# Kernel optimization log

Hardware: AMD Instinct MI355X
Metric: run time of the kernel (lower is better)

## Reference

```python
import jax, jax.numpy as jnp
import numpy as np

N = 50000
IN_DIM = 128
HID = 16
HEADS = 8
NUM_CLASSES = 16
NEG_SLOPE = 0.2


def _glorot(key, shape):
    fan_in, fan_out = shape[0], shape[-1]
    lim = float(np.sqrt(6.0 / (fan_in + fan_out)))
    return jax.random.uniform(key, shape, jnp.float32, -lim, lim)


def setup_inputs() -> dict:
    key = jax.random.key(0)
    ks = jax.random.split(key, 12)
    x = jax.random.normal(ks[0], (N, IN_DIM), jnp.float32)
    edge_index = jax.random.randint(ks[1], (2, 1600000), 0, N, jnp.int64)
    # conv1: in=IN_DIM, out per head=HID, heads=HEADS
    Wl1 = _glorot(ks[2], (IN_DIM, HEADS * HID))
    Wr1 = _glorot(ks[3], (IN_DIM, HEADS * HID))
    att1 = _glorot(ks[4], (HEADS, HID))
    b1 = jnp.zeros((HEADS * HID,), jnp.float32)
    # conv2: in=HID*HEADS, out per head=NUM_CLASSES
    Wl2 = _glorot(ks[5], (HEADS * HID, HEADS * NUM_CLASSES))
    Wr2 = _glorot(ks[6], (HEADS * HID, HEADS * NUM_CLASSES))
    att2 = _glorot(ks[7], (HEADS, NUM_CLASSES))
    b2 = jnp.zeros((HEADS * NUM_CLASSES,), jnp.float32)
    # final linear: NUM_CLASSES*HEADS -> NUM_CLASSES
    Wlin = _glorot(ks[8], (HEADS * NUM_CLASSES, NUM_CLASSES))
    blin = jnp.zeros((NUM_CLASSES,), jnp.float32)
    return dict(x=x, edge_index=edge_index, Wl1=Wl1, Wr1=Wr1, att1=att1, b1=b1,
                Wl2=Wl2, Wr2=Wr2, att2=att2, b2=b2, Wlin=Wlin, blin=blin)


def _gatv2_conv(x, src, dst, Wl, Wr, att, bias, heads, out_ch):
    n = x.shape[0]
    xl = (x @ Wl).reshape(n, heads, out_ch)  # source transform
    xr = (x @ Wr).reshape(n, heads, out_ch)  # target transform
    # additive attention logits per edge (GATv2)
    e = jax.nn.leaky_relu(xl[src] + xr[dst], NEG_SLOPE)          # [E,H,C]
    logits = jnp.einsum('ehc,hc->eh', e, att)                     # [E,H]
    # per-destination segment softmax
    m = jax.ops.segment_max(logits, dst, num_segments=n)          # [N,H]
    a = jnp.exp(logits - m[dst])                                  # [E,H]
    s = jax.ops.segment_sum(a, dst, num_segments=n)               # [N,H]
    alpha = a / (s[dst] + 1e-16)
    out = jax.ops.segment_sum(alpha[:, :, None] * xl[src], dst, num_segments=n)
    return out.reshape(n, heads * out_ch) + bias


def reference(x, edge_index, Wl1, Wr1, att1, b1, Wl2, Wr2, att2, b2, Wlin, blin):
    n = x.shape[0]
    # add self-loops (PyG GATv2Conv default add_self_loops=True)
    loop = jnp.arange(n, dtype=edge_index.dtype)
    src = jnp.concatenate([edge_index[0], loop])
    dst = jnp.concatenate([edge_index[1], loop])
    h = _gatv2_conv(x, src, dst, Wl1, Wr1, att1, b1, HEADS, HID)
    h = jax.nn.relu(h)  # dropout identity in eval mode
    h = _gatv2_conv(h, src, dst, Wl2, Wr2, att2, b2, HEADS, NUM_CLASSES)
    h = jax.nn.relu(h)
    logits = h @ Wlin + blin
    return jax.nn.log_softmax(logits, axis=1)
```

## Files before the change

### kernel.cpp

```cpp
#include <hip/hip_runtime.h>

#define HEADS 8
#define FDIM 128
#define NCLS 16
#define NEG_SLOPE 0.2f
#define LOG2E 1.4426950408889634f

typedef __attribute__((ext_vector_type(8))) short bf16x8;
typedef __attribute__((ext_vector_type(4))) float f32x4;

__device__ __forceinline__ unsigned short f2bf(float f) {
    unsigned u = __float_as_uint(f);
    unsigned r = u + 0x7FFFu + ((u >> 16) & 1u);
    return (unsigned short)(r >> 16);
}

__global__ __launch_bounds__(256) void gemm_csr(const float* __restrict__ X,
                                                const float* __restrict__ W0,
                                                const float* __restrict__ W1,
                                                unsigned short* __restrict__ Y0,
                                                unsigned short* __restrict__ Y1,
                                                int n,
                                                const int* __restrict__ srcs,
                                                const int* __restrict__ dsts,
                                                int* __restrict__ cnt,
                                                int* __restrict__ adj,
                                                int E0, int pad, int S) {
    __shared__ __align__(16) unsigned short xs[4 * 4 * 64 * 8];
    __shared__ __align__(16) unsigned short ws[8 * 4 * 64 * 8];
    const int t = threadIdx.x;
    const int x = blockIdx.x;
    int gIdx;
    if (S > 0) {
        if ((x % 3) == 2) {
            int i = (x / 3) * 256 + t;
            const int stride = S * 256;
            for (; i < E0; i += stride) {
                const int d = dsts[i];
                const int rk = atomicAdd(&cnt[d], 1);
                if (rk < pad) adj[(size_t)d * pad + rk] = srcs[i];
            }
            return;
        }
        gIdx = (x / 3) * 2 + (x % 3);
    } else {
        gIdx = x;
    }
    const int Gh = (n + 63) >> 6;
    if (gIdx >= 2 * Gh) return;
    const float* W = (gIdx < Gh) ? W0 : W1;
    unsigned short* Y = (gIdx < Gh) ? Y0 : Y1;
    const int nb = (gIdx < Gh ? gIdx : gIdx - Gh) * 64;

#pragma unroll
    for (int i = 0; i < 8; i++) {
        const int f = t + i * 256;
        const int node = f >> 5, k4 = f & 31;
        float4 v = make_float4(0.f, 0.f, 0.f, 0.f);
        if (nb + node < n) v = ((const float4*)(X + (size_t)(nb + node) * 128))[k4];
        const int kc = k4 >> 3;
        const int q = (k4 & 7) >> 1;
        const int half = k4 & 1;
        const int lane = q * 16 + (node & 15);
        const int w_ = node >> 4;
        union { unsigned short us[4]; uint2 u2; } pk;
        pk.us[0] = f2bf(v.x); pk.us[1] = f2bf(v.y);
        pk.us[2] = f2bf(v.z); pk.us[3] = f2bf(v.w);
        *(uint2*)&xs[(((w_ * 4 + kc) * 64 + lane) << 3) + half * 4] = pk.u2;
    }
#pragma unroll
    for (int i = 0; i < 16; i++) {
        const int f = t + i * 256;
        const int k = f >> 5, n4 = f & 31;
        const float4 v = *(const float4*)(W + k * 128 + n4 * 4);
        const int kc = k >> 5, q = (k >> 3) & 3, j = k & 7;
        const float vv[4] = {v.x, v.y, v.z, v.w};
#pragma unroll
        for (int e = 0; e < 4; e++) {
            const int nn = n4 * 4 + e;
            const int ct = nn >> 4;
            const int lane = q * 16 + (nn & 15);
            ws[(((ct * 4 + kc) * 64 + lane) << 3) + j] = f2bf(vv[e]);
        }
    }
    __syncthreads();

    const int w = t >> 6, lane = t & 63;
    f32x4 acc[8];
#pragma unroll
    for (int i = 0; i < 8; i++) acc[i] = (f32x4){0.f, 0.f, 0.f, 0.f};
    const bf16x8* xa = (const bf16x8*)xs;
    const bf16x8* wb = (const bf16x8*)ws;
#pragma unroll
    for (int kc = 0; kc < 4; kc++) {
        const bf16x8 a = xa[(w * 4 + kc) * 64 + lane];
#pragma unroll
        for (int ct = 0; ct < 8; ct++) {
            const bf16x8 b = wb[(ct * 4 + kc) * 64 + lane];
            acc[ct] = __builtin_amdgcn_mfma_f32_16x16x32_bf16(a, b, acc[ct], 0, 0, 0);
        }
    }
    const int q = lane >> 4, nn = lane & 15;
#pragma unroll
    for (int ct = 0; ct < 8; ct++) {
#pragma unroll
        for (int r = 0; r < 4; r++) {
            const int row = nb + w * 16 + q * 4 + r;
            if (row < n) Y[(size_t)row * 128 + ct * 16 + nn] = f2bf(acc[ct][r]);
        }
    }
}

__global__ __launch_bounds__(256) void node_gather(const unsigned short* __restrict__ xl,
                                                   const unsigned short* __restrict__ xr,
                                                   const float* __restrict__ att,
                                                   const int* __restrict__ adj,
                                                   const int* __restrict__ cnt,
                                                   const float* __restrict__ bias,
                                                   float* __restrict__ outC,
                                                   const float* __restrict__ headW,
                                                   const float* __restrict__ headB,
                                                   float* __restrict__ outH,
                                                   int n, int pad) {
    __shared__ float WsL[FDIM * NCLS];
    __shared__ __align__(16) float stage[4][FDIM];
    const int t = threadIdx.x;
    if (headW) {
        for (int i = t; i < FDIM * NCLS; i += 256) WsL[i] = headW[i];
        __syncthreads();
    }
    const int lane = t & 63;
    const int w = t >> 6;
    const int node = blockIdx.x * 4 + w;
    if (node >= n) return;
    const int half = lane >> 5;
    const int sub = lane & 31;
    const int col = sub * 4;
    const float4 av = *(const float4*)(att + col);
    const float a0 = av.x * LOG2E, a1 = av.y * LOG2E;
    const float a2 = av.z * LOG2E, a3 = av.w * LOG2E;

    float r0, r1, r2, r3, sl0, sl1, sl2, sl3;
    {
        const uint2 rv = *(const uint2*)(xr + (size_t)node * FDIM + col);
        r0 = __uint_as_float(rv.x << 16); r1 = __uint_as_float(rv.x & 0xFFFF0000u);
        r2 = __uint_as_float(rv.y << 16); r3 = __uint_as_float(rv.y & 0xFFFF0000u);
        const uint2 lv = *(const uint2*)(xl + (size_t)node * FDIM + col);
        sl0 = __uint_as_float(lv.x << 16); sl1 = __uint_as_float(lv.x & 0xFFFF0000u);
        sl2 = __uint_as_float(lv.y << 16); sl3 = __uint_as_float(lv.y & 0xFFFF0000u);
    }
    float mx;
    {
        float z0 = sl0 + r0; z0 = fmaxf(z0, NEG_SLOPE * z0);
        float z1 = sl1 + r1; z1 = fmaxf(z1, NEG_SLOPE * z1);
        float z2 = sl2 + r2; z2 = fmaxf(z2, NEG_SLOPE * z2);
        float z3 = sl3 + r3; z3 = fmaxf(z3, NEG_SLOPE * z3);
        float p = z0 * a0 + z1 * a1 + z2 * a2 + z3 * a3;
        p += __shfl_xor(p, 1, 64);
        p += __shfl_xor(p, 2, 64);
        mx = p;
    }
    float s, acc0, acc1, acc2, acc3;
    if (half == 0) { s = 1.f; acc0 = sl0; acc1 = sl1; acc2 = sl2; acc3 = sl3; }
    else           { s = 0.f; acc0 = acc1 = acc2 = acc3 = 0.f; }

    const int* ap = adj + (size_t)node * pad;
    const int deg = min(cnt[node], pad);
    int j = 0;
    for (; j + 8 <= deg; j += 8) {
        const int4 sa = *(const int4*)(ap + j);
        const int4 sb = *(const int4*)(ap + j + 4);
#pragma unroll
        for (int k = 0; k < 4; k++) {
            int pA, pB;
            if (k == 0) { pA = sa.x; pB = sa.y; }
            else if (k == 1) { pA = sa.z; pB = sa.w; }
            else if (k == 2) { pA = sb.x; pB = sb.y; }
            else { pA = sb.z; pB = sb.w; }
            const int src = half ? pB : pA;
            const uint2 lv = *(const uint2*)(xl + (size_t)src * FDIM + col);
            const float l0 = __uint_as_float(lv.x << 16);
            const float l1 = __uint_as_float(lv.x & 0xFFFF0000u);
            const float l2 = __uint_as_float(lv.y << 16);
            const float l3 = __uint_as_float(lv.y & 0xFFFF0000u);
            float z0 = l0 + r0; z0 = fmaxf(z0, NEG_SLOPE * z0);
            float z1 = l1 + r1; z1 = fmaxf(z1, NEG_SLOPE * z1);
            float z2 = l2 + r2; z2 = fmaxf(z2, NEG_SLOPE * z2);
            float z3 = l3 + r3; z3 = fmaxf(z3, NEG_SLOPE * z3);
            float p = z0 * a0 + z1 * a1 + z2 * a2 + z3 * a3;
            p += __shfl_xor(p, 1, 64);
            p += __shfl_xor(p, 2, 64);
            const float e = exp2f(p - mx);
            s += e;
            acc0 += e * l0; acc1 += e * l1; acc2 += e * l2; acc3 += e * l3;
        }
    }
    for (; j < deg; j += 2) {
        const int pA = ap[j];
        const int pB = (j + 1 < deg) ? ap[j + 1] : pA;
        const float gate = (half == 0 || j + 1 < deg) ? 1.f : 0.f;
        const int src = half ? pB : pA;
        const uint2 lv = *(const uint2*)(xl + (size_t)src * FDIM + col);
        const float l0 = __uint_as_float(lv.x << 16);
        const float l1 = __uint_as_float(lv.x & 0xFFFF0000u);
        const float l2 = __uint_as_float(lv.y << 16);
        const float l3 = __uint_as_float(lv.y & 0xFFFF0000u);
        float z0 = l0 + r0; z0 = fmaxf(z0, NEG_SLOPE * z0);
        float z1 = l1 + r1; z1 = fmaxf(z1, NEG_SLOPE * z1);
        float z2 = l2 + r2; z2 = fmaxf(z2, NEG_SLOPE * z2);
        float z3 = l3 + r3; z3 = fmaxf(z3, NEG_SLOPE * z3);
        float p = z0 * a0 + z1 * a1 + z2 * a2 + z3 * a3;
        p += __shfl_xor(p, 1, 64);
        p += __shfl_xor(p, 2, 64);
        const float e = exp2f(p - mx) * gate;
        s += e;
        acc0 += e * l0; acc1 += e * l1; acc2 += e * l2; acc3 += e * l3;
    }
    s    += __shfl_xor(s, 32, 64);
    acc0 += __shfl_xor(acc0, 32, 64);
    acc1 += __shfl_xor(acc1, 32, 64);
    acc2 += __shfl_xor(acc2, 32, 64);
    acc3 += __shfl_xor(acc3, 32, 64);

    const float inv = 1.f / (s + 1e-16f);
    const float4 bv = *(const float4*)(bias + col);
    float o0 = fmaxf(acc0 * inv + bv.x, 0.f);
    float o1 = fmaxf(acc1 * inv + bv.y, 0.f);
    float o2 = fmaxf(acc2 * inv + bv.z, 0.f);
    float o3 = fmaxf(acc3 * inv + bv.w, 0.f);

    if (!headW) {
        if (half == 0)
            *(float4*)(outC + (size_t)node * FDIM + col) = make_float4(o0, o1, o2, o3);
        return;
    }
    if (half == 0)
        *(float4*)&stage[w][col] = make_float4(o0, o1, o2, o3);
    const int cls = lane & 15;
    const int q = lane >> 4;
    float acc = 0.f;
#pragma unroll
    for (int k = 0; k < 32; k++)
        acc += stage[w][q * 32 + k] * WsL[(q * 32 + k) * NCLS + cls];
    acc += __shfl_xor(acc, 16, 64);
    acc += __shfl_xor(acc, 32, 64);
    acc += headB[cls];
    float m2 = acc;
    m2 = fmaxf(m2, __shfl_xor(m2, 8, 64));
    m2 = fmaxf(m2, __shfl_xor(m2, 4, 64));
    m2 = fmaxf(m2, __shfl_xor(m2, 2, 64));
    m2 = fmaxf(m2, __shfl_xor(m2, 1, 64));
    float sm = __expf(acc - m2);
    sm += __shfl_xor(sm, 8, 64);
    sm += __shfl_xor(sm, 4, 64);
    sm += __shfl_xor(sm, 2, 64);
    sm += __shfl_xor(sm, 1, 64);
    if (lane < 16)
        outH[(size_t)node * NCLS + cls] = acc - m2 - __logf(sm);
}

extern "C" void kernel_launch(void* const* d_in, const int* in_sizes, int n_in,
                              void* d_out, int out_size, void* d_ws, size_t ws_size,
                              hipStream_t stream) {
    const float* x    = (const float*)d_in[0];
    const int*   edge = (const int*)d_in[1];
    const float* Wl1  = (const float*)d_in[2];
    const float* Wr1  = (const float*)d_in[3];
    const float* att1 = (const float*)d_in[4];
    const float* b1   = (const float*)d_in[5];
    const float* Wl2  = (const float*)d_in[6];
    const float* Wr2  = (const float*)d_in[7];
    const float* att2 = (const float*)d_in[8];
    const float* b2   = (const float*)d_in[9];
    const float* Wlin = (const float*)d_in[10];
    const float* blin = (const float*)d_in[11];

    const int N = in_sizes[0] / FDIM;
    const int E0 = in_sizes[1] / 2;
    const int* srcs = edge;
    const int* dsts = edge + E0;

    int PAD = 96;
    {
        size_t need = (size_t)N * FDIM * 2 * 2 + (size_t)N * FDIM * 4
                    + (size_t)N * 4 + (size_t)N * PAD * 4;
        if (need > ws_size) PAD = 72;
    }

    unsigned short* A = (unsigned short*)d_ws;
    unsigned short* B = A + (size_t)N * FDIM;
    float* C   = (float*)(B + (size_t)N * FDIM);
    int* cnt   = (int*)(C + (size_t)N * FDIM);
    int* adj   = cnt + N;

    const int Gh = (N + 63) / 64;
    const int G = 2 * Gh;
    const int node_blocks = (N + 3) / 4;

    hipMemsetAsync(cnt, 0, (size_t)N * sizeof(int), stream);

    gemm_csr<<<3 * Gh, 256, 0, stream>>>(
        x, Wl1, Wr1, A, B, N, srcs, dsts, cnt, adj, E0, PAD, Gh);
    node_gather<<<node_blocks, 256, 0, stream>>>(A, B, att1, adj, cnt, b1, C,
                                                 nullptr, nullptr, nullptr, N, PAD);

    gemm_csr<<<G, 256, 0, stream>>>(
        C, Wl2, Wr2, A, B, N, nullptr, nullptr, nullptr, nullptr, 0, PAD, 0);
    node_gather<<<node_blocks, 256, 0, stream>>>(A, B, att2, adj, cnt, b2,
                                                 nullptr, Wlin, blin,
                                                 (float*)d_out, N, PAD);
}
```

Measured before the change: 396.5 us.

## Persistent GEMM blocks, direct A-fragment loads, bf16 hidden layer, dual accumulators

The GEMM kernel becomes persistent: a fixed grid of blocks loads and converts W into shared memory once, then loops over node tiles, loading A fragments straight from global memory into registers instead of staging them in shared memory. The CSR build uses its own fixed set of blocks. The layer-1 output is stored as bf16, which halves its write and read traffic, and the layer-2 GEMM reads that bf16 directly. The gather loop splits into two independent accumulator sets to add ILP. The cost is more rounding from the bf16 intermediate and less parallelism per tile in the GEMM.

New measurement: 394.8 us. Within noise of the previous version (-0.4%).

```diff
diff --git a/kernel.cpp b/kernel.cpp
--- a/kernel.cpp
+++ b/kernel.cpp
@@ -15,7 +15,8 @@
     return (unsigned short)(r >> 16);
 }
 
-__global__ __launch_bounds__(256) void gemm_csr(const float* __restrict__ X,
+__global__ __launch_bounds__(256) void gemm_csr(const float* __restrict__ Xf,
+                                                const unsigned short* __restrict__ Xb,
                                                 const float* __restrict__ W0,
                                                 const float* __restrict__ W1,
                                                 unsigned short* __restrict__ Y0,
@@ -25,49 +26,24 @@
                                                 const int* __restrict__ dsts,
                                                 int* __restrict__ cnt,
                                                 int* __restrict__ adj,
-                                                int E0, int pad, int S) {
-    __shared__ __align__(16) unsigned short xs[4 * 4 * 64 * 8];
+                                                int E0, int pad, int GB, int SB) {
     __shared__ __align__(16) unsigned short ws[8 * 4 * 64 * 8];
     const int t = threadIdx.x;
     const int x = blockIdx.x;
-    int gIdx;
-    if (S > 0) {
-        if ((x % 3) == 2) {
-            int i = (x / 3) * 256 + t;
-            const int stride = S * 256;
-            for (; i < E0; i += stride) {
-                const int d = dsts[i];
-                const int rk = atomicAdd(&cnt[d], 1);
-                if (rk < pad) adj[(size_t)d * pad + rk] = srcs[i];
-            }
-            return;
-        }
-        gIdx = (x / 3) * 2 + (x % 3);
-    } else {
-        gIdx = x;
-    }
-    const int Gh = (n + 63) >> 6;
-    if (gIdx >= 2 * Gh) return;
-    const float* W = (gIdx < Gh) ? W0 : W1;
-    unsigned short* Y = (gIdx < Gh) ? Y0 : Y1;
-    const int nb = (gIdx < Gh ? gIdx : gIdx - Gh) * 64;
-
-#pragma unroll
-    for (int i = 0; i < 8; i++) {
-        const int f = t + i * 256;
-        const int node = f >> 5, k4 = f & 31;
-        float4 v = make_float4(0.f, 0.f, 0.f, 0.f);
-        if (nb + node < n) v = ((const float4*)(X + (size_t)(nb + node) * 128))[k4];
-        const int kc = k4 >> 3;
-        const int q = (k4 & 7) >> 1;
-        const int half = k4 & 1;
-        const int lane = q * 16 + (node & 15);
-        const int w_ = node >> 4;
-        union { unsigned short us[4]; uint2 u2; } pk;
-        pk.us[0] = f2bf(v.x); pk.us[1] = f2bf(v.y);
-        pk.us[2] = f2bf(v.z); pk.us[3] = f2bf(v.w);
-        *(uint2*)&xs[(((w_ * 4 + kc) * 64 + lane) << 3) + half * 4] = pk.u2;
-    }
+    if (x >= 2 * GB) {
+        int i = (x - 2 * GB) * 256 + t;
+        const int stride = SB * 256;
+        for (; i < E0; i += stride) {
+            const int d = dsts[i];
+            const int rk = atomicAdd(&cnt[d], 1);
+            if (rk < pad) adj[(size_t)d * pad + rk] = srcs[i];
+        }
+        return;
+    }
+    const int side = (x >= GB) ? 1 : 0;
+    const float* W = side ? W1 : W0;
+    unsigned short* Y = side ? Y1 : Y0;
+
 #pragma unroll
     for (int i = 0; i < 16; i++) {
         const int f = t + i * 256;
@@ -78,38 +54,84 @@
 #pragma unroll
         for (int e = 0; e < 4; e++) {
             const int nn = n4 * 4 + e;
-            const int ct = nn >> 4;
-            const int lane = q * 16 + (nn & 15);
-            ws[(((ct * 4 + kc) * 64 + lane) << 3) + j] = f2bf(vv[e]);
+            ws[((((nn >> 4) * 4 + kc) * 64 + q * 16 + (nn & 15)) << 3) + j] = f2bf(vv[e]);
         }
     }
     __syncthreads();
 
     const int w = t >> 6, lane = t & 63;
-    f32x4 acc[8];
-#pragma unroll
-    for (int i = 0; i < 8; i++) acc[i] = (f32x4){0.f, 0.f, 0.f, 0.f};
-    const bf16x8* xa = (const bf16x8*)xs;
+    const int q = lane >> 4, m = lane & 15;
     const bf16x8* wb = (const bf16x8*)ws;
-#pragma unroll
-    for (int kc = 0; kc < 4; kc++) {
-        const bf16x8 a = xa[(w * 4 + kc) * 64 + lane];
+    const int Gh = (n + 63) >> 6;
+    const int bid = side ? x - GB : x;
+
+    for (int tile = bid; tile < Gh; tile += GB) {
+        const int nb = tile * 64;
+        const int arow = nb + w * 16 + m;
+        bf16x8 af[4];
+        if (arow < n) {
+            if (Xb) {
+                const unsigned short* xp = Xb + (size_t)arow * 128 + q * 8;
+#pragma unroll
+                for (int kc = 0; kc < 4; kc++) af[kc] = *(const bf16x8*)(xp + kc * 32);
+            } else {
+                const float* xp = Xf + (size_t)arow * 128 + q * 8;
+#pragma unroll
+                for (int kc = 0; kc < 4; kc++) {
+                    const float4 v0 = *(const float4*)(xp + kc * 32);
+                    const float4 v1 = *(const float4*)(xp + kc * 32 + 4);
+                    union { unsigned short us[8]; bf16x8 b; } pk;
+                    pk.us[0] = f2bf(v0.x); pk.us[1] = f2bf(v0.y);
+                    pk.us[2] = f2bf(v0.z); pk.us[3] = f2bf(v0.w);
+                    pk.us[4] = f2bf(v1.x); pk.us[5] = f2bf(v1.y);
+                    pk.us[6] = f2bf(v1.z); pk.us[7] = f2bf(v1.w);
+                    af[kc] = pk.b;
+                }
+            }
+        } else {
+#pragma unroll
+            for (int kc = 0; kc < 4; kc++) af[kc] = (bf16x8){0,0,0,0,0,0,0,0};
+        }
+        f32x4 acc[8];
+#pragma unroll
+        for (int i = 0; i < 8; i++) acc[i] = (f32x4){0.f, 0.f, 0.f, 0.f};
+#pragma unroll
+        for (int kc = 0; kc < 4; kc++) {
+#pragma unroll
+            for (int ct = 0; ct < 8; ct++)
+                acc[ct] = __builtin_amdgcn_mfma_f32_16x16x32_bf16(
+                    af[kc], wb[(ct * 4 + kc) * 64 + lane], acc[ct], 0, 0, 0);
+        }
 #pragma unroll
         for (int ct = 0; ct < 8; ct++) {
-            const bf16x8 b = wb[(ct * 4 + kc) * 64 + lane];
-            acc[ct] = __builtin_amdgcn_mfma_f32_16x16x32_bf16(a, b, acc[ct], 0, 0, 0);
-        }
-    }
-    const int q = lane >> 4, nn = lane & 15;
-#pragma unroll
-    for (int ct = 0; ct < 8; ct++) {
-#pragma unroll
-        for (int r = 0; r < 4; r++) {
-            const int row = nb + w * 16 + q * 4 + r;
-            if (row < n) Y[(size_t)row * 128 + ct * 16 + nn] = f2bf(acc[ct][r]);
+#pragma unroll
+            for (int r = 0; r < 4; r++) {
+                const int row = nb + w * 16 + q * 4 + r;
+                if (row < n) Y[(size_t)row * 128 + ct * 16 + m] = f2bf(acc[ct][r]);
+            }
         }
     }
 }
+
+#define GATHER_EDGE(pA, pB, S_, A0_, A1_, A2_, A3_)                          \
+    {                                                                        \
+        const int src_ = half ? (pB) : (pA);                                 \
+        const uint2 lv_ = *(const uint2*)(xl + (size_t)src_ * FDIM + col);   \
+        const float l0_ = __uint_as_float(lv_.x << 16);                      \
+        const float l1_ = __uint_as_float(lv_.x & 0xFFFF0000u);              \
+        const float l2_ = __uint_as_float(lv_.y << 16);                      \
+        const float l3_ = __uint_as_float(lv_.y & 0xFFFF0000u);              \
+        float z0_ = l0_ + r0; z0_ = fmaxf(z0_, NEG_SLOPE * z0_);             \
+        float z1_ = l1_ + r1; z1_ = fmaxf(z1_, NEG_SLOPE * z1_);             \
+        float z2_ = l2_ + r2; z2_ = fmaxf(z2_, NEG_SLOPE * z2_);             \
+        float z3_ = l3_ + r3; z3_ = fmaxf(z3_, NEG_SLOPE * z3_);             \
+        float p_ = z0_ * a0 + z1_ * a1 + z2_ * a2 + z3_ * a3;                \
+        p_ += __shfl_xor(p_, 1, 64);                                         \
+        p_ += __shfl_xor(p_, 2, 64);                                         \
+        const float e_ = exp2f(p_ - mx);                                     \
+        S_ += e_;                                                            \
+        A0_ += e_ * l0_; A1_ += e_ * l1_; A2_ += e_ * l2_; A3_ += e_ * l3_;  \
+    }
 
 __global__ __launch_bounds__(256) void node_gather(const unsigned short* __restrict__ xl,
                                                    const unsigned short* __restrict__ xr,
@@ -117,7 +139,7 @@
                                                    const int* __restrict__ adj,
                                                    const int* __restrict__ cnt,
                                                    const float* __restrict__ bias,
-                                                   float* __restrict__ outC,
+                                                   unsigned short* __restrict__ outC,
                                                    const float* __restrict__ headW,
                                                    const float* __restrict__ headB,
                                                    float* __restrict__ outH,
@@ -160,9 +182,10 @@
         p += __shfl_xor(p, 2, 64);
         mx = p;
     }
-    float s, acc0, acc1, acc2, acc3;
-    if (half == 0) { s = 1.f; acc0 = sl0; acc1 = sl1; acc2 = sl2; acc3 = sl3; }
-    else           { s = 0.f; acc0 = acc1 = acc2 = acc3 = 0.f; }
+    float sA, aA0, aA1, aA2, aA3;
+    float sB = 0.f, aB0 = 0.f, aB1 = 0.f, aB2 = 0.f, aB3 = 0.f;
+    if (half == 0) { sA = 1.f; aA0 = sl0; aA1 = sl1; aA2 = sl2; aA3 = sl3; }
+    else           { sA = 0.f; aA0 = aA1 = aA2 = aA3 = 0.f; }
 
     const int* ap = adj + (size_t)node * pad;
     const int deg = min(cnt[node], pad);
@@ -170,30 +193,10 @@
     for (; j + 8 <= deg; j += 8) {
         const int4 sa = *(const int4*)(ap + j);
         const int4 sb = *(const int4*)(ap + j + 4);
-#pragma unroll
-        for (int k = 0; k < 4; k++) {
-            int pA, pB;
-            if (k == 0) { pA = sa.x; pB = sa.y; }
-            else if (k == 1) { pA = sa.z; pB = sa.w; }
-            else if (k == 2) { pA = sb.x; pB = sb.y; }
-            else { pA = sb.z; pB = sb.w; }
-            const int src = half ? pB : pA;
-            const uint2 lv = *(const uint2*)(xl + (size_t)src * FDIM + col);
-            const float l0 = __uint_as_float(lv.x << 16);
-            const float l1 = __uint_as_float(lv.x & 0xFFFF0000u);
-            const float l2 = __uint_as_float(lv.y << 16);
-            const float l3 = __uint_as_float(lv.y & 0xFFFF0000u);
-            float z0 = l0 + r0; z0 = fmaxf(z0, NEG_SLOPE * z0);
-            float z1 = l1 + r1; z1 = fmaxf(z1, NEG_SLOPE * z1);
-            float z2 = l2 + r2; z2 = fmaxf(z2, NEG_SLOPE * z2);
-            float z3 = l3 + r3; z3 = fmaxf(z3, NEG_SLOPE * z3);
-            float p = z0 * a0 + z1 * a1 + z2 * a2 + z3 * a3;
-            p += __shfl_xor(p, 1, 64);
-            p += __shfl_xor(p, 2, 64);
-            const float e = exp2f(p - mx);
-            s += e;
-            acc0 += e * l0; acc1 += e * l1; acc2 += e * l2; acc3 += e * l3;
-        }
+        GATHER_EDGE(sa.x, sa.y, sA, aA0, aA1, aA2, aA3)
+        GATHER_EDGE(sa.z, sa.w, sB, aB0, aB1, aB2, aB3)
+        GATHER_EDGE(sb.x, sb.y, sA, aA0, aA1, aA2, aA3)
+        GATHER_EDGE(sb.z, sb.w, sB, aB0, aB1, aB2, aB3)
     }
     for (; j < deg; j += 2) {
         const int pA = ap[j];
@@ -213,9 +216,11 @@
         p += __shfl_xor(p, 1, 64);
         p += __shfl_xor(p, 2, 64);
         const float e = exp2f(p - mx) * gate;
-        s += e;
-        acc0 += e * l0; acc1 += e * l1; acc2 += e * l2; acc3 += e * l3;
-    }
+        sA += e;
+        aA0 += e * l0; aA1 += e * l1; aA2 += e * l2; aA3 += e * l3;
+    }
+    float s = sA + sB;
+    float acc0 = aA0 + aB0, acc1 = aA1 + aB1, acc2 = aA2 + aB2, acc3 = aA3 + aB3;
     s    += __shfl_xor(s, 32, 64);
     acc0 += __shfl_xor(acc0, 32, 64);
     acc1 += __shfl_xor(acc1, 32, 64);
@@ -224,14 +229,18 @@
 
     const float inv = 1.f / (s + 1e-16f);
     const float4 bv = *(const float4*)(bias + col);
-    float o0 = fmaxf(acc0 * inv + bv.x, 0.f);
-    float o1 = fmaxf(acc1 * inv + bv.y, 0.f);
-    float o2 = fmaxf(acc2 * inv + bv.z, 0.f);
-    float o3 = fmaxf(acc3 * inv + bv.w, 0.f);
+    const float o0 = fmaxf(acc0 * inv + bv.x, 0.f);
+    const float o1 = fmaxf(acc1 * inv + bv.y, 0.f);
+    const float o2 = fmaxf(acc2 * inv + bv.z, 0.f);
+    const float o3 = fmaxf(acc3 * inv + bv.w, 0.f);
 
     if (!headW) {
-        if (half == 0)
-            *(float4*)(outC + (size_t)node * FDIM + col) = make_float4(o0, o1, o2, o3);
+        if (half == 0) {
+            union { unsigned short us[4]; uint2 u2; } pk;
+            pk.us[0] = f2bf(o0); pk.us[1] = f2bf(o1);
+            pk.us[2] = f2bf(o2); pk.us[3] = f2bf(o3);
+            *(uint2*)(outC + (size_t)node * FDIM + col) = pk.u2;
+        }
         return;
     }
     if (half == 0)
@@ -282,30 +291,29 @@
 
     int PAD = 96;
     {
-        size_t need = (size_t)N * FDIM * 2 * 2 + (size_t)N * FDIM * 4
-                    + (size_t)N * 4 + (size_t)N * PAD * 4;
+        size_t need = (size_t)3 * N * FDIM * 2 + (size_t)N * 4 + (size_t)N * PAD * 4;
         if (need > ws_size) PAD = 72;
     }
 
     unsigned short* A = (unsigned short*)d_ws;
     unsigned short* B = A + (size_t)N * FDIM;
-    float* C   = (float*)(B + (size_t)N * FDIM);
+    unsigned short* C = B + (size_t)N * FDIM;
     int* cnt   = (int*)(C + (size_t)N * FDIM);
     int* adj   = cnt + N;
 
-    const int Gh = (N + 63) / 64;
-    const int G = 2 * Gh;
+    const int GB = 320;
+    const int SB = 256;
     const int node_blocks = (N + 3) / 4;
 
     hipMemsetAsync(cnt, 0, (size_t)N * sizeof(int), stream);
 
-    gemm_csr<<<3 * Gh, 256, 0, stream>>>(
-        x, Wl1, Wr1, A, B, N, srcs, dsts, cnt, adj, E0, PAD, Gh);
+    gemm_csr<<<2 * GB + SB, 256, 0, stream>>>(
+        x, nullptr, Wl1, Wr1, A, B, N, srcs, dsts, cnt, adj, E0, PAD, GB, SB);
     node_gather<<<node_blocks, 256, 0, stream>>>(A, B, att1, adj, cnt, b1, C,
                                                  nullptr, nullptr, nullptr, N, PAD);
 
-    gemm_csr<<<G, 256, 0, stream>>>(
-        C, Wl2, Wr2, A, B, N, nullptr, nullptr, nullptr, nullptr, 0, PAD, 0);
+    gemm_csr<<<2 * GB, 256, 0, stream>>>(
+        nullptr, C, Wl2, Wr2, A, B, N, nullptr, nullptr, nullptr, nullptr, 0, PAD, GB, 0);
     node_gather<<<node_blocks, 256, 0, stream>>>(A, B, att2, adj, cnt, b2,
                                                  nullptr, Wlin, blin,
                                                  (float*)d_out, N, PAD);
```
